# Optimization experiments

Measured on AMD Instinct MI355X. Metric: run time of the kernel, lower is better.

The kernel has to match this reference:

```python
import jax, jax.numpy as jnp
import numpy as np

K = 7            # attention window
HEADS = 8
C_ATT = 32       # in_channels of AttBlock
DKH = C_ATT // HEADS  # 4
C_FC = 512       # resnet18 fc channels
NUM_CLASS = 20


def conv2d(x, w, b, stride=1, padding=0):
    out = jax.lax.conv_general_dilated(
        x, w, (stride, stride), [(padding, padding), (padding, padding)],
        dimension_numbers=("NCHW", "OIHW", "NCHW"))
    return out + b[None, :, None, None]


def unfold2(t, k, H, W):
    # torch t.unfold(2,k,1).unfold(3,k,1): [B,C,Hp,Wp] -> [B,C,H,W,k,k]
    t = jnp.stack([t[:, :, i:i + H, :] for i in range(k)], axis=-1)      # [B,C,H,Wp,k]
    t = jnp.stack([t[:, :, :, j:j + W, :] for j in range(k)], axis=-1)   # [B,C,H,W,k,k]
    return t


def bilinear_resize(x, oh, ow):
    # torch F.interpolate(mode='bilinear', align_corners=False)
    B, C, H, W = x.shape
    ys = jnp.clip((jnp.arange(oh, dtype=x.dtype) + 0.5) * (H / oh) - 0.5, 0, H - 1)
    xs = jnp.clip((jnp.arange(ow, dtype=x.dtype) + 0.5) * (W / ow) - 0.5, 0, W - 1)
    y0 = jnp.floor(ys).astype(jnp.int32); y1 = jnp.minimum(y0 + 1, H - 1)
    x0 = jnp.floor(xs).astype(jnp.int32); x1 = jnp.minimum(x0 + 1, W - 1)
    wy = (ys - y0)[None, None, :, None]
    wx = (xs - x0)[None, None, None, :]
    g = lambda yi, xi: x[:, :, yi][:, :, :, xi]
    top = g(y0, x0) * (1 - wx) + g(y0, x1) * wx
    bot = g(y1, x0) * (1 - wx) + g(y1, x1) * wx
    return top * (1 - wy) + bot * wy


def att_block(x, conv1_w, conv1_b, k_w, k_b, q_w, q_b, v_w, v_b, rel_h, rel_w):
    B, _, H, W = x.shape
    x1 = conv2d(x, conv1_w, conv1_b, padding=1)                    # [B,32,H,W]
    p = (K - 1) // 2
    xp = jnp.pad(x1, ((0, 0), (0, 0), (p, K - 1 - p), (p, K - 1 - p)))
    k = conv2d(xp, k_w, k_b)                                       # [B,32,H+6,W+6]
    q = conv2d(x1, q_w, q_b)                                       # [B,32,H,W]
    v = conv2d(xp, v_w, v_b)
    k = unfold2(k, K, H, W).reshape(B, HEADS, H, W, DKH, -1)       # raw row-major reshape (as torch)
    v = unfold2(v, K, H, W).reshape(B, HEADS, H, W, DKH, -1)
    q = q.reshape(B, HEADS, H, W, DKH, 1)
    qk = jnp.matmul(jnp.swapaxes(q, 4, 5), k).reshape(B, HEADS, H, W, K, K)
    # einsum 'bhxydz,cij->bhxyij' fully contracts d,z,c -> outer product of sums
    qsum = q.sum(axis=(4, 5))                                      # [B,heads,H,W]
    rel = rel_h.sum(0) + rel_w.sum(0)                              # [K,1]+[1,K] -> [K,K]
    qk = qk + qsum[..., None, None] * rel
    w = jax.nn.softmax(qk.reshape(B, HEADS, H, W, 1, K * K), axis=-1)
    attn = jnp.matmul(w, jnp.swapaxes(v, 4, 5))                    # [B,heads,H,W,1,dvh]
    return attn.reshape(B, -1, H, W)                               # [B,32,H,W]


def setup_inputs() -> dict:
    key = jax.random.key(0)
    ks = jax.random.split(key, 16)
    s = 0.05
    inp = {
        "x": jax.random.normal(ks[0], (1, 6, 256, 256), jnp.float32),
        "diff_input": 1,
        "backbone_w": jax.random.normal(ks[1], (C_FC, 6, 3, 3), jnp.float32) * s,
        "backbone_b": jax.random.normal(ks[2], (C_FC,), jnp.float32) * s,
        "conv1_w": jax.random.normal(ks[3], (C_ATT, 6, 3, 3), jnp.float32) * s,
        "conv1_b": jax.random.normal(ks[4], (C_ATT,), jnp.float32) * s,
        "k_w": jax.random.normal(ks[5], (C_ATT, C_ATT, 1, 1), jnp.float32) * s,
        "k_b": jax.random.normal(ks[6], (C_ATT,), jnp.float32) * s,
        "q_w": jax.random.normal(ks[7], (C_ATT, C_ATT, 1, 1), jnp.float32) * s,
        "q_b": jax.random.normal(ks[8], (C_ATT,), jnp.float32) * s,
        "v_w": jax.random.normal(ks[9], (C_ATT, C_ATT, 1, 1), jnp.float32) * s,
        "v_b": jax.random.normal(ks[10], (C_ATT,), jnp.float32) * s,
        "rel_h": jax.random.normal(ks[11], (C_ATT // 2, K, 1), jnp.float32),
        "rel_w": jax.random.normal(ks[12], (C_ATT // 2, 1, K), jnp.float32),
        "expand_w": jax.random.normal(ks[13], (C_FC, C_ATT, 3, 3), jnp.float32) * s,
        "expand_b": jax.random.normal(ks[14], (C_FC,), jnp.float32) * s,
        "fc_w": jax.random.normal(ks[15], (NUM_CLASS, C_FC), jnp.float32) * s,
        "fc_b": jnp.zeros((NUM_CLASS,), jnp.float32),
    }
    return inp


def reference(x, diff_input, backbone_w, backbone_b, conv1_w, conv1_b,
              k_w, k_b, q_w, q_b, v_w, v_b, rel_h, rel_w,
              expand_w, expand_b, fc_w, fc_b):
    # multi_task_model stub: stride-8 conv trunk -> [B,512,H/8,W/8]
    res_out = conv2d(x, backbone_w, backbone_b, stride=8, padding=1)
    # diff_input is not None -> attention branch always taken
    att_res = att_block(x, conv1_w, conv1_b, k_w, k_b, q_w, q_b, v_w, v_b, rel_h, rel_w)
    att_scale = bilinear_resize(att_res, res_out.shape[2], res_out.shape[3])
    att_enhance = res_out + conv2d(att_scale, expand_w, expand_b, padding=1)
    pooled = att_enhance.mean(axis=(2, 3))          # AdaptiveAvgPool2d((1,1))
    fc_x = pooled @ fc_w.T + fc_b                   # [B,num_class]
    return fc_x
```

## Files before the change

kernel.cpp:

```cpp
#include <hip/hip_runtime.h>
#include <math.h>


#define OFF_STATA ((size_t)0)
#define OFF_SX    ((size_t)3072)
#define OFF_G     ((size_t)3136)
#define OFF_GB    ((size_t)8896)
#define OFF_FCB2  ((size_t)9976)

#define SM_KT   0
#define SM_VT   2176
#define SM_QS   4352
#define SM_ML   4864
#define SM_BIAS 5032
#define SM_RW   5040
#define SM_RED  5056
#define SM_TOT  5120

__global__ __launch_bounds__(256) void k_fused(
    const float* __restrict__ x,
    const float* __restrict__ c1w, const float* __restrict__ c1b,
    const float* __restrict__ kw, const float* __restrict__ kb,
    const float* __restrict__ qw, const float* __restrict__ qb,
    const float* __restrict__ vw, const float* __restrict__ vb,
    const float* __restrict__ relh, const float* __restrict__ relw,
    const float* __restrict__ bw, const float* __restrict__ bb,
    const float* __restrict__ ew, const float* __restrict__ eb,
    const float* __restrict__ fcw, const float* __restrict__ fcb,
    float* __restrict__ statA, float* __restrict__ Sx,
    float* __restrict__ G, float* __restrict__ Gb,
    float* __restrict__ FCB2) {
  __shared__ float smem[SM_TOT];
  int tid = threadIdx.x;
  int bid = blockIdx.x;

  if (bid >= 1024) {
    float* red2 = smem;
    if (bid < 1078) {
      int e = bid - 1024;
      int ci = e / 9, rem = e - ci * 9, ky = rem / 3, kx = rem - ky * 3;
      const float* xc = x + (size_t)ci * 65536;
      float acc = 0.f;
      for (int p = tid; p < 1024; p += 256) {
        int oy = p >> 5, ox = p & 31;
        int ry = 8 * oy - 1 + ky, cx = 8 * ox - 1 + kx;
        if (ry >= 0 && ry <= 255 && cx >= 0 && cx <= 255)
          acc += xc[ry * 256 + cx];
      }
      #pragma unroll
      for (int off = 32; off >= 1; off >>= 1) acc += __shfl_down(acc, off);
      if ((tid & 63) == 0) red2[tid >> 6] = acc;
      __syncthreads();
      if (tid == 0) Sx[e] = red2[0] + red2[1] + red2[2] + red2[3];
      return;
    }
    if (bid < 1185) {
      int gi0 = (bid - 1078) * 64;
      int l = tid & 63, w = tid >> 6;
      int g = gi0 + l;
      int o = g / 342;
      int i = g - o * 342;
      bool valid = (g < 6840);
      int oc = valid ? o : 0;
      float acc = 0.f;
      const float* fr = fcw + oc * 512;
      #pragma unroll 8
      for (int mm = 0; mm < 128; ++mm) {
        int m = w * 128 + mm;
        float val = (i < 288) ? ew[m * 288 + i] : bw[m * 54 + (i - 288)];
        acc = fmaf(fr[m], val, acc);
      }
      red2[tid] = acc;
      __syncthreads();
      if (w == 0 && valid) {
        float s = red2[l] + red2[64 + l] + red2[128 + l] + red2[192 + l];
        if (i < 288) G[o * 288 + i] = s;
        else         Gb[o * 54 + (i - 288)] = s;
      }
      return;
    }
    {
      int o = bid - 1185;
      float acc = fmaf(fcw[o * 512 + tid], bb[tid] + eb[tid],
                       fcw[o * 512 + 256 + tid] * (bb[256 + tid] + eb[256 + tid]));
      #pragma unroll
      for (int off = 32; off >= 1; off >>= 1) acc += __shfl_down(acc, off);
      if ((tid & 63) == 0) red2[tid >> 6] = acc;
      __syncthreads();
      if (tid == 0) FCB2[o] = fcb[o] + red2[0] + red2[1] + red2[2] + red2[3];
      return;
    }
  }

  int c  = bid >> 5;
  int oy = bid & 31;

  float* KT  = smem + SM_KT;
  float* VT  = smem + SM_VT;
  float* QS  = smem + SM_QS;
  float* Ml  = smem + SM_ML;
  float* bsl = smem + SM_BIAS;
  float* rhs = smem + SM_RW;
  float* rws = smem + SM_RW + 8;
  float* red = smem + SM_RED;

  if (tid < 168) {
    int ci = tid / 28, s = tid - ci * 28;
    if (s < 27) {
      int kind = s / 9, t9 = s - kind * 9;
      const float* w3 = (kind == 0 ? kw : (kind == 1 ? vw : qw)) + c * 32;
      float a = 0.f;
      #pragma unroll
      for (int m = 0; m < 32; ++m)
        a = fmaf(w3[m], c1w[(m * 6 + ci) * 9 + t9], a);
      Ml[ci * 28 + s] = a;
    }
  } else if (tid < 176) {
    int s = tid - 168;
    if (s < 3) {
      const float* w3 = (s == 0 ? kw : (s == 1 ? vw : qw)) + c * 32;
      float a = (s == 0 ? kb : (s == 1 ? vb : qb))[c];
      #pragma unroll
      for (int m = 0; m < 32; ++m) a = fmaf(w3[m], c1b[m], a);
      bsl[s] = a;
    } else if (s == 3) bsl[3] = kb[c];
    else if (s == 4) bsl[4] = vb[c];
  } else if (tid < 184) {
    int i = tid - 176;
    if (i < 7) {
      float s = 0.f;
      for (int cc = 0; cc < 16; ++cc) s += relh[cc * 7 + i];
      rhs[i] = s;
    }
  } else if (tid < 192) {
    int j = tid - 184;
    if (j < 7) {
      float s = 0.f;
      for (int cc = 0; cc < 16; ++cc) s += relw[cc * 7 + j];
      rws[j] = s;
    }
  }
  __syncthreads();

  int cg = tid & 63, rg = tid >> 6;
  int roq = (rg == 1) ? 1 : ((rg == 2) ? 0 : -1);
  float kacc[2][4], vacc[2][4], qacc[4];
  {
    float mk = bsl[0], mv = bsl[1], mq = bsl[2];
    #pragma unroll
    for (int ro = 0; ro < 2; ++ro)
      #pragma unroll
      for (int cc = 0; cc < 4; ++cc) { kacc[ro][cc] = mk; vacc[ro][cc] = mv; }
    #pragma unroll
    for (int cc = 0; cc < 4; ++cc) qacc[cc] = mq;
  }
  float mA = (cg > 0) ? 1.0f : 0.0f;
  float mC = (cg < 63) ? 1.0f : 0.0f;
  int xr0 = 8 * oy + 2 * rg - 1;

  #pragma unroll 1
  for (int ci = 0; ci < 6; ++ci) {
    const float* xch = x + (size_t)ci * 65536;
    float wch[28];
    {
      const float4* Mc = (const float4*)&Ml[ci * 28];
      *(float4*)&wch[0]  = Mc[0]; *(float4*)&wch[4]  = Mc[1];
      *(float4*)&wch[8]  = Mc[2]; *(float4*)&wch[12] = Mc[3];
      *(float4*)&wch[16] = Mc[4]; *(float4*)&wch[20] = Mc[5];
      *(float4*)&wch[24] = Mc[6];
    }
    #pragma unroll
    for (int s4 = 0; s4 < 4; ++s4) {
      int xr = xr0 + s4;
      if (xr < 0 || xr > 255) continue;
      float4 Bv = *(const float4*)&xch[xr * 256 + 4 * cg];
      float left  = __shfl_up(Bv.w, 1);
      float right = __shfl_down(Bv.x, 1);
      float win[6];
      win[0] = left * mA;
      win[1] = Bv.x;
      win[2] = Bv.y;
      win[3] = Bv.z;
      win[4] = Bv.w;
      win[5] = right * mC;
      if (s4 < 3) {
        const float* wk = &wch[3 * s4];
        const float* wv = &wch[9 + 3 * s4];
        #pragma unroll
        for (int cc = 0; cc < 4; ++cc) {
          float a = kacc[0][cc], b2 = vacc[0][cc];
          #pragma unroll
          for (int dxw = 0; dxw < 3; ++dxw) {
            float xv = win[cc + dxw];
            a  = fmaf(wk[dxw], xv, a);
            b2 = fmaf(wv[dxw], xv, b2);
          }
          kacc[0][cc] = a; vacc[0][cc] = b2;
        }
        if (roq == 0) {
          const float* wq = &wch[18 + 3 * s4];
          #pragma unroll
          for (int cc = 0; cc < 4; ++cc) {
            float qa = qacc[cc];
            #pragma unroll
            for (int dxw = 0; dxw < 3; ++dxw)
              qa = fmaf(wq[dxw], win[cc + dxw], qa);
            qacc[cc] = qa;
          }
        }
      }
      if (s4 >= 1) {
        const float* wk = &wch[3 * (s4 - 1)];
        const float* wv = &wch[9 + 3 * (s4 - 1)];
        #pragma unroll
        for (int cc = 0; cc < 4; ++cc) {
          float a = kacc[1][cc], b2 = vacc[1][cc];
          #pragma unroll
          for (int dxw = 0; dxw < 3; ++dxw) {
            float xv = win[cc + dxw];
            a  = fmaf(wk[dxw], xv, a);
            b2 = fmaf(wv[dxw], xv, b2);
          }
          kacc[1][cc] = a; vacc[1][cc] = b2;
        }
        if (roq == 1) {
          const float* wq = &wch[18 + 3 * (s4 - 1)];
          #pragma unroll
          for (int cc = 0; cc < 4; ++cc) {
            float qa = qacc[cc];
            #pragma unroll
            for (int dxw = 0; dxw < 3; ++dxw)
              qa = fmaf(wq[dxw], win[cc + dxw], qa);
            qacc[cc] = qa;
          }
        }
      }
    }
  }

  #pragma unroll
  for (int ro = 0; ro < 2; ++ro) {
    int r = 2 * rg + ro;
    *(float4*)&KT[r * 272 + 4 * cg + 4] =
        make_float4(kacc[ro][0], kacc[ro][1], kacc[ro][2], kacc[ro][3]);
    *(float4*)&VT[r * 272 + 4 * cg + 4] =
        make_float4(vacc[ro][0], vacc[ro][1], vacc[ro][2], vacc[ro][3]);
  }
  if (roq >= 0)
    *(float4*)&QS[(rg == 2 ? 256 : 0) + 4 * cg] =
        make_float4(qacc[0], qacc[1], qacc[2], qacc[3]);
  if (tid < 96) {
    int t2 = tid;
    int kv = t2 >= 48; if (kv) t2 -= 48;
    int lr = t2 & 7, pi = t2 >> 3;
    int slot = (pi < 3) ? (pi + 1) : (pi + 257);
    (kv ? VT : KT)[lr * 272 + slot] = bsl[3 + kv];
  }
  __syncthreads();

  {
    int half = tid & 1;
    int pix  = tid >> 1;
    int dx   = pix & 1;
    int ox   = (pix >> 1) & 31;
    int dy   = (pix >> 6) & 1;
    int wb   = 8 * ox + 4 * dx;
    int dv   = dx ? 0 : 3;
    int i0   = half * 3;

    float4 qv4 = *(const float4*)&QS[dy * 256 + wb];
    float qv0 = qv4.x, qv1 = qv4.y, qv2 = qv4.z, qv3 = qv4.w;
    float qsum = qv0 + qv1 + qv2 + qv3;

    float sum = 0.f, o = 0.f;
    #pragma unroll
    for (int ii = 0; ii < 4; ++ii) {
      int i = i0 + ii;
      float act = ((half == 0) || (ii > 0)) ? 1.0f : 0.0f;
      const float* kr = &KT[(dy + i) * 272 + wb];
      const float* vr = &VT[(dy + i) * 272 + wb];
      float B[12], BV[12];
      *(float4*)&B[0]  = *(const float4*)&kr[0];
      *(float4*)&B[4]  = *(const float4*)&kr[4];
      *(float4*)&B[8]  = *(const float4*)&kr[8];
      *(float4*)&BV[0] = *(const float4*)&vr[0];
      *(float4*)&BV[4] = *(const float4*)&vr[4];
      *(float4*)&BV[8] = *(const float4*)&vr[8];
      float rh = rhs[i];
      #pragma unroll
      for (int j = 0; j < 7; ++j) {
        float d0 = fmaf(qv0, B[j + 1],
                   fmaf(qv1, B[j + 2],
                   fmaf(qv2, B[j + 3], qv3 * B[j + 4])));
        float s = fmaf(qsum, rh + rws[j], d0);
        float e = act * __expf(s);
        sum += e;
        o = fmaf(e, BV[dv + j + 1], o);
      }
    }
    sum += __shfl_xor(sum, 1);
    o   += __shfl_xor(o, 1);

    float quarter = 0.25f * o / sum;
    float psum = quarter + __shfl_xor(quarter, 2);
    if ((tid & 3) == 0) red[dy * 32 + ox] = psum;
  }
  __syncthreads();

  if (tid < 32) {
    float scv = red[tid] + red[32 + tid];
    float e0  = __shfl(scv, 0, 32);
    float e31 = __shfl(scv, 31, 32);
    float rs = scv;
    #pragma unroll
    for (int off = 16; off >= 1; off >>= 1) rs += __shfl_down(rs, off, 32);
    if (tid == 0) {
      float* pa = statA + (c * 32 + oy) * 3;
      pa[0] = rs; pa[1] = e0; pa[2] = e31;
    }
  }
}

__global__ __launch_bounds__(64) void k_out(
    const float* __restrict__ statA, const float* __restrict__ Sx,
    const float* __restrict__ G, const float* __restrict__ Gb,
    const float* __restrict__ FCB2, float* __restrict__ out) {
  __shared__ float Sl[288];
  __shared__ float SxL[54];
  int o = blockIdx.x, lane = threadIdx.x;
  if (lane < 32) {
    int ch = lane;
    const float* pa = statA + ch * 96;
    float T = 0.f, C0 = 0.f, C31 = 0.f;
    #pragma unroll
    for (int i = 0; i < 32; ++i) {
      T += pa[3 * i]; C0 += pa[3 * i + 1]; C31 += pa[3 * i + 2];
    }
    float r0 = pa[0],  e00 = pa[1],    e0_31 = pa[2];
    float r31 = pa[93], e31_0 = pa[94], e31_31 = pa[95];
    #pragma unroll
    for (int ky = 0; ky < 3; ++ky) {
      float exR = (ky == 0) ? r31 : (ky == 2 ? r0 : 0.f);
      #pragma unroll
      for (int kx = 0; kx < 3; ++kx) {
        float exC = (kx == 0) ? C31 : (kx == 2 ? C0 : 0.f);
        float corner = 0.f;
        if (ky != 1 && kx != 1) {
          if (ky == 0) corner = (kx == 0) ? e31_31 : e31_0;
          else         corner = (kx == 0) ? e0_31  : e00;
        }
        Sl[ch * 9 + ky * 3 + kx] = T - exR - exC + corner;
      }
    }
  } else {
    for (int idx = lane - 32; idx < 54; idx += 32) SxL[idx] = Sx[idx];
  }
  __syncthreads();

  float acc = 0.f;
  #pragma unroll
  for (int i0 = 0; i0 < 288; i0 += 64) {
    int i = i0 + lane;
    if (i < 288) acc = fmaf(G[o * 288 + i], Sl[i], acc);
  }
  if (lane < 54) acc = fmaf(Gb[o * 54 + lane], SxL[lane], acc);
  #pragma unroll
  for (int off = 32; off >= 1; off >>= 1) acc += __shfl_down(acc, off);
  if (lane == 0) out[o] = FCB2[o] + acc * (1.0f / 1024.0f);
}

extern "C" void kernel_launch(void* const* d_in, const int* in_sizes, int n_in,
                              void* d_out, int out_size, void* d_ws, size_t ws_size,
                              hipStream_t stream) {
  const float* x    = (const float*)d_in[0];
  const float* bw   = (const float*)d_in[2];
  const float* bb   = (const float*)d_in[3];
  const float* c1w  = (const float*)d_in[4];
  const float* c1b  = (const float*)d_in[5];
  const float* kw   = (const float*)d_in[6];
  const float* kb   = (const float*)d_in[7];
  const float* qw   = (const float*)d_in[8];
  const float* qb   = (const float*)d_in[9];
  const float* vw   = (const float*)d_in[10];
  const float* vb   = (const float*)d_in[11];
  const float* relh = (const float*)d_in[12];
  const float* relw = (const float*)d_in[13];
  const float* ew   = (const float*)d_in[14];
  const float* eb   = (const float*)d_in[15];
  const float* fcw  = (const float*)d_in[16];
  const float* fcb  = (const float*)d_in[17];

  float* ws    = (float*)d_ws;
  float* statA = ws + OFF_STATA;
  float* Sxb   = ws + OFF_SX;
  float* Gm    = ws + OFF_G;
  float* Gbm   = ws + OFF_GB;
  float* FCB2  = ws + OFF_FCB2;
  float* out   = (float*)d_out;

  k_fused<<<1205, 256, 0, stream>>>(x, c1w, c1b, kw, kb, qw, qb, vw, vb,
                                    relh, relw, bw, bb, ew, eb, fcw, fcb,
                                    statA, Sxb, Gm, Gbm, FCB2);
  k_out  <<<20,   64,  0, stream>>>(statA, Sxb, Gm, Gbm, FCB2, out);
}
```

Before: 29.79 us.

## Double block size to 512 threads, one conv row per wavefront

Raises the fused kernel to 512 threads per block. In the conv phase each wavefront now computes one K/V row instead of two, which removes the two-accumulator register pattern. In the attention phase four threads now share each pixel's window rows instead of two. The shared-memory row stride changes from 272 to 276 and the auxiliary blocks are adjusted for eight waves. The aim is more parallelism per block and fewer serial FMAs per thread. In exchange, neighbouring conv rows now each reload the same input rows, and every block carries more synchronisation and reduction overhead.

```diff
diff --git a/kernel.cpp b/kernel.cpp
--- a/kernel.cpp
+++ b/kernel.cpp
@@ -9,15 +9,15 @@
 #define OFF_FCB2  ((size_t)9976)
 
 #define SM_KT   0
-#define SM_VT   2176
-#define SM_QS   4352
-#define SM_ML   4864
-#define SM_BIAS 5032
-#define SM_RW   5040
-#define SM_RED  5056
-#define SM_TOT  5120
-
-__global__ __launch_bounds__(256) void k_fused(
+#define SM_VT   2208
+#define SM_QS   4416
+#define SM_ML   4928
+#define SM_BIAS 5096
+#define SM_RW   5104
+#define SM_RED  5120
+#define SM_TOT  5184
+
+__global__ __launch_bounds__(512) void k_fused(
     const float* __restrict__ x,
     const float* __restrict__ c1w, const float* __restrict__ c1b,
     const float* __restrict__ kw, const float* __restrict__ kb,
@@ -41,7 +41,7 @@
       int ci = e / 9, rem = e - ci * 9, ky = rem / 3, kx = rem - ky * 3;
       const float* xc = x + (size_t)ci * 65536;
       float acc = 0.f;
-      for (int p = tid; p < 1024; p += 256) {
+      for (int p = tid; p < 1024; p += 512) {
         int oy = p >> 5, ox = p & 31;
         int ry = 8 * oy - 1 + ky, cx = 8 * ox - 1 + kx;
         if (ry >= 0 && ry <= 255 && cx >= 0 && cx <= 255)
@@ -51,7 +51,12 @@
       for (int off = 32; off >= 1; off >>= 1) acc += __shfl_down(acc, off);
       if ((tid & 63) == 0) red2[tid >> 6] = acc;
       __syncthreads();
-      if (tid == 0) Sx[e] = red2[0] + red2[1] + red2[2] + red2[3];
+      if (tid == 0) {
+        float s = 0.f;
+        #pragma unroll
+        for (int wv2 = 0; wv2 < 8; ++wv2) s += red2[wv2];
+        Sx[e] = s;
+      }
       return;
     }
     if (bid < 1185) {
@@ -65,15 +70,17 @@
       float acc = 0.f;
       const float* fr = fcw + oc * 512;
       #pragma unroll 8
-      for (int mm = 0; mm < 128; ++mm) {
-        int m = w * 128 + mm;
+      for (int mm = 0; mm < 64; ++mm) {
+        int m = w * 64 + mm;
         float val = (i < 288) ? ew[m * 288 + i] : bw[m * 54 + (i - 288)];
         acc = fmaf(fr[m], val, acc);
       }
       red2[tid] = acc;
       __syncthreads();
       if (w == 0 && valid) {
-        float s = red2[l] + red2[64 + l] + red2[128 + l] + red2[192 + l];
+        float s = 0.f;
+        #pragma unroll
+        for (int wv2 = 0; wv2 < 8; ++wv2) s += red2[wv2 * 64 + l];
         if (i < 288) G[o * 288 + i] = s;
         else         Gb[o * 54 + (i - 288)] = s;
       }
@@ -81,13 +88,17 @@
     }
     {
       int o = bid - 1185;
-      float acc = fmaf(fcw[o * 512 + tid], bb[tid] + eb[tid],
-                       fcw[o * 512 + 256 + tid] * (bb[256 + tid] + eb[256 + tid]));
+      float acc = fcw[o * 512 + tid] * (bb[tid] + eb[tid]);
       #pragma unroll
       for (int off = 32; off >= 1; off >>= 1) acc += __shfl_down(acc, off);
       if ((tid & 63) == 0) red2[tid >> 6] = acc;
       __syncthreads();
-      if (tid == 0) FCB2[o] = fcb[o] + red2[0] + red2[1] + red2[2] + red2[3];
+      if (tid == 0) {
+        float s = fcb[o];
+        #pragma unroll
+        for (int wv2 = 0; wv2 < 8; ++wv2) s += red2[wv2];
+        FCB2[o] = s;
+      }
       return;
     }
   }
@@ -142,21 +153,17 @@
   }
   __syncthreads();
 
-  int cg = tid & 63, rg = tid >> 6;
-  int roq = (rg == 1) ? 1 : ((rg == 2) ? 0 : -1);
-  float kacc[2][4], vacc[2][4], qacc[4];
+  int cg = tid & 63, r = tid >> 6;
+  bool isq = (r == 3 || r == 4);
+  float kacc[4], vacc[4], qacc[4];
   {
     float mk = bsl[0], mv = bsl[1], mq = bsl[2];
     #pragma unroll
-    for (int ro = 0; ro < 2; ++ro)
-      #pragma unroll
-      for (int cc = 0; cc < 4; ++cc) { kacc[ro][cc] = mk; vacc[ro][cc] = mv; }
-    #pragma unroll
-    for (int cc = 0; cc < 4; ++cc) qacc[cc] = mq;
+    for (int cc = 0; cc < 4; ++cc) { kacc[cc] = mk; vacc[cc] = mv; qacc[cc] = mq; }
   }
   float mA = (cg > 0) ? 1.0f : 0.0f;
   float mC = (cg < 63) ? 1.0f : 0.0f;
-  int xr0 = 8 * oy + 2 * rg - 1;
+  int xrbase = 8 * oy + r - 1;
 
   #pragma unroll 1
   for (int ci = 0; ci < 6; ++ci) {
@@ -170,8 +177,8 @@
       *(float4*)&wch[24] = Mc[6];
     }
     #pragma unroll
-    for (int s4 = 0; s4 < 4; ++s4) {
-      int xr = xr0 + s4;
+    for (int dy = 0; dy < 3; ++dy) {
+      int xr = xrbase + dy;
       if (xr < 0 || xr > 255) continue;
       float4 Bv = *(const float4*)&xch[xr * 256 + 4 * cg];
       float left  = __shfl_up(Bv.w, 1);
@@ -183,90 +190,58 @@
       win[3] = Bv.z;
       win[4] = Bv.w;
       win[5] = right * mC;
-      if (s4 < 3) {
-        const float* wk = &wch[3 * s4];
-        const float* wv = &wch[9 + 3 * s4];
+      const float* wk = &wch[3 * dy];
+      const float* wv = &wch[9 + 3 * dy];
+      #pragma unroll
+      for (int cc = 0; cc < 4; ++cc) {
+        float a = kacc[cc], b2 = vacc[cc];
+        #pragma unroll
+        for (int dxw = 0; dxw < 3; ++dxw) {
+          float xv = win[cc + dxw];
+          a  = fmaf(wk[dxw], xv, a);
+          b2 = fmaf(wv[dxw], xv, b2);
+        }
+        kacc[cc] = a; vacc[cc] = b2;
+      }
+      if (isq) {
+        const float* wq = &wch[18 + 3 * dy];
         #pragma unroll
         for (int cc = 0; cc < 4; ++cc) {
-          float a = kacc[0][cc], b2 = vacc[0][cc];
+          float qa = qacc[cc];
           #pragma unroll
-          for (int dxw = 0; dxw < 3; ++dxw) {
-            float xv = win[cc + dxw];
-            a  = fmaf(wk[dxw], xv, a);
-            b2 = fmaf(wv[dxw], xv, b2);
-          }
-          kacc[0][cc] = a; vacc[0][cc] = b2;
+          for (int dxw = 0; dxw < 3; ++dxw)
+            qa = fmaf(wq[dxw], win[cc + dxw], qa);
+          qacc[cc] = qa;
         }
-        if (roq == 0) {
-          const float* wq = &wch[18 + 3 * s4];
-          #pragma unroll
-          for (int cc = 0; cc < 4; ++cc) {
-            float qa = qacc[cc];
-            #pragma unroll
-            for (int dxw = 0; dxw < 3; ++dxw)
-              qa = fmaf(wq[dxw], win[cc + dxw], qa);
-            qacc[cc] = qa;
-          }
-        }
-      }
-      if (s4 >= 1) {
-        const float* wk = &wch[3 * (s4 - 1)];
-        const float* wv = &wch[9 + 3 * (s4 - 1)];
-        #pragma unroll
-        for (int cc = 0; cc < 4; ++cc) {
-          float a = kacc[1][cc], b2 = vacc[1][cc];
-          #pragma unroll
-          for (int dxw = 0; dxw < 3; ++dxw) {
-            float xv = win[cc + dxw];
-            a  = fmaf(wk[dxw], xv, a);
-            b2 = fmaf(wv[dxw], xv, b2);
-          }
-          kacc[1][cc] = a; vacc[1][cc] = b2;
-        }
-        if (roq == 1) {
-          const float* wq = &wch[18 + 3 * (s4 - 1)];
-          #pragma unroll
-          for (int cc = 0; cc < 4; ++cc) {
-            float qa = qacc[cc];
-            #pragma unroll
-            for (int dxw = 0; dxw < 3; ++dxw)
-              qa = fmaf(wq[dxw], win[cc + dxw], qa);
-            qacc[cc] = qa;
-          }
-        }
-      }
-    }
-  }
-
-  #pragma unroll
-  for (int ro = 0; ro < 2; ++ro) {
-    int r = 2 * rg + ro;
-    *(float4*)&KT[r * 272 + 4 * cg + 4] =
-        make_float4(kacc[ro][0], kacc[ro][1], kacc[ro][2], kacc[ro][3]);
-    *(float4*)&VT[r * 272 + 4 * cg + 4] =
-        make_float4(vacc[ro][0], vacc[ro][1], vacc[ro][2], vacc[ro][3]);
-  }
-  if (roq >= 0)
-    *(float4*)&QS[(rg == 2 ? 256 : 0) + 4 * cg] =
-        make_float4(qacc[0], qacc[1], qacc[2], qacc[3]);
+      }
+    }
+  }
+
+  *(float4*)&KT[r * 276 + 4 * cg + 4] =
+      make_float4(kacc[0], kacc[1], kacc[2], kacc[3]);
+  *(float4*)&VT[r * 276 + 4 * cg + 4] =
+      make_float4(vacc[0], vacc[1], vacc[2], vacc[3]);
+  if (r == 3)
+    *(float4*)&QS[4 * cg] = make_float4(qacc[0], qacc[1], qacc[2], qacc[3]);
+  if (r == 4)
+    *(float4*)&QS[256 + 4 * cg] = make_float4(qacc[0], qacc[1], qacc[2], qacc[3]);
   if (tid < 96) {
     int t2 = tid;
     int kv = t2 >= 48; if (kv) t2 -= 48;
     int lr = t2 & 7, pi = t2 >> 3;
     int slot = (pi < 3) ? (pi + 1) : (pi + 257);
-    (kv ? VT : KT)[lr * 272 + slot] = bsl[3 + kv];
+    (kv ? VT : KT)[lr * 276 + slot] = bsl[3 + kv];
   }
   __syncthreads();
 
   {
-    int half = tid & 1;
-    int pix  = tid >> 1;
+    int quarter = tid & 3;
+    int pix  = tid >> 2;
     int dx   = pix & 1;
     int ox   = (pix >> 1) & 31;
     int dy   = (pix >> 6) & 1;
     int wb   = 8 * ox + 4 * dx;
     int dv   = dx ? 0 : 3;
-    int i0   = half * 3;
 
     float4 qv4 = *(const float4*)&QS[dy * 256 + wb];
     float qv0 = qv4.x, qv1 = qv4.y, qv2 = qv4.z, qv3 = qv4.w;
@@ -274,11 +249,12 @@
 
     float sum = 0.f, o = 0.f;
     #pragma unroll
-    for (int ii = 0; ii < 4; ++ii) {
-      int i = i0 + ii;
-      float act = ((half == 0) || (ii > 0)) ? 1.0f : 0.0f;
-      const float* kr = &KT[(dy + i) * 272 + wb];
-      const float* vr = &VT[(dy + i) * 272 + wb];
+    for (int ii = 0; ii < 2; ++ii) {
+      int i = quarter + 4 * ii;
+      float act = (i < 7) ? 1.0f : 0.0f;
+      int irow = (i < 7) ? i : 0;
+      const float* kr = &KT[(dy + irow) * 276 + wb];
+      const float* vr = &VT[(dy + irow) * 276 + wb];
       float B[12], BV[12];
       *(float4*)&B[0]  = *(const float4*)&kr[0];
       *(float4*)&B[4]  = *(const float4*)&kr[4];
@@ -286,7 +262,7 @@
       *(float4*)&BV[0] = *(const float4*)&vr[0];
       *(float4*)&BV[4] = *(const float4*)&vr[4];
       *(float4*)&BV[8] = *(const float4*)&vr[8];
-      float rh = rhs[i];
+      float rh = rhs[irow];
       #pragma unroll
       for (int j = 0; j < 7; ++j) {
         float d0 = fmaf(qv0, B[j + 1],
@@ -300,10 +276,12 @@
     }
     sum += __shfl_xor(sum, 1);
     o   += __shfl_xor(o, 1);
-
-    float quarter = 0.25f * o / sum;
-    float psum = quarter + __shfl_xor(quarter, 2);
-    if ((tid & 3) == 0) red[dy * 32 + ox] = psum;
+    sum += __shfl_xor(sum, 2);
+    o   += __shfl_xor(o, 2);
+
+    float quarterv = 0.25f * o / sum;
+    float psum = quarterv + __shfl_xor(quarterv, 4);
+    if ((tid & 7) == 0) red[dy * 32 + ox] = psum;
   }
   __syncthreads();
 
@@ -398,7 +376,7 @@
   float* FCB2  = ws + OFF_FCB2;
   float* out   = (float*)d_out;
 
-  k_fused<<<1205, 256, 0, stream>>>(x, c1w, c1b, kw, kb, qw, qb, vw, vb,
+  k_fused<<<1205, 512, 0, stream>>>(x, c1w, c1b, kw, kb, qw, qb, vw, vb,
                                     relh, relw, bw, bb, ew, eb, fcw, fcb,
                                     statA, Sxb, Gm, Gbm, FCB2);
   k_out  <<<20,   64,  0, stream>>>(statA, Sxb, Gm, Gbm, FCB2, out);
```

Result: slower. 31.35 us (+5.2%).

## Fuse final output kernel into main kernel via last-block atomic counter

Applied to the files above, without the earlier changes.

Removes the separate k_out launch. Each block of k_fused now increments a global counter after a threadfence, and the last block to finish does the final reduction over statA, Sx, G and Gb for all 20 outputs. This saves a kernel launch and the gap between kernels. In exchange it adds a memset before the launch, an atomic and fences in every block, and a serialized tail on one block.

```diff
diff --git a/kernel.cpp b/kernel.cpp
--- a/kernel.cpp
+++ b/kernel.cpp
@@ -7,6 +7,7 @@
 #define OFF_G     ((size_t)3136)
 #define OFF_GB    ((size_t)8896)
 #define OFF_FCB2  ((size_t)9976)
+#define OFF_CNT   ((size_t)10000)
 
 #define SM_KT   0
 #define SM_VT   2176
@@ -29,8 +30,10 @@
     const float* __restrict__ fcw, const float* __restrict__ fcb,
     float* __restrict__ statA, float* __restrict__ Sx,
     float* __restrict__ G, float* __restrict__ Gb,
-    float* __restrict__ FCB2) {
+    float* __restrict__ FCB2, unsigned int* __restrict__ cnt,
+    float* __restrict__ out) {
   __shared__ float smem[SM_TOT];
+  __shared__ unsigned int rankS;
   int tid = threadIdx.x;
   int bid = blockIdx.x;
 
@@ -52,9 +55,7 @@
       if ((tid & 63) == 0) red2[tid >> 6] = acc;
       __syncthreads();
       if (tid == 0) Sx[e] = red2[0] + red2[1] + red2[2] + red2[3];
-      return;
-    }
-    if (bid < 1185) {
+    } else if (bid < 1185) {
       int gi0 = (bid - 1078) * 64;
       int l = tid & 63, w = tid >> 6;
       int g = gi0 + l;
@@ -77,9 +78,7 @@
         if (i < 288) G[o * 288 + i] = s;
         else         Gb[o * 54 + (i - 288)] = s;
       }
-      return;
-    }
-    {
+    } else {
       int o = bid - 1185;
       float acc = fmaf(fcw[o * 512 + tid], bb[tid] + eb[tid],
                        fcw[o * 512 + 256 + tid] * (bb[256 + tid] + eb[256 + tid]));
@@ -88,248 +87,248 @@
       if ((tid & 63) == 0) red2[tid >> 6] = acc;
       __syncthreads();
       if (tid == 0) FCB2[o] = fcb[o] + red2[0] + red2[1] + red2[2] + red2[3];
-      return;
-    }
-  }
-
-  int c  = bid >> 5;
-  int oy = bid & 31;
-
-  float* KT  = smem + SM_KT;
-  float* VT  = smem + SM_VT;
-  float* QS  = smem + SM_QS;
-  float* Ml  = smem + SM_ML;
-  float* bsl = smem + SM_BIAS;
-  float* rhs = smem + SM_RW;
-  float* rws = smem + SM_RW + 8;
-  float* red = smem + SM_RED;
-
-  if (tid < 168) {
-    int ci = tid / 28, s = tid - ci * 28;
-    if (s < 27) {
-      int kind = s / 9, t9 = s - kind * 9;
-      const float* w3 = (kind == 0 ? kw : (kind == 1 ? vw : qw)) + c * 32;
-      float a = 0.f;
-      #pragma unroll
-      for (int m = 0; m < 32; ++m)
-        a = fmaf(w3[m], c1w[(m * 6 + ci) * 9 + t9], a);
-      Ml[ci * 28 + s] = a;
-    }
-  } else if (tid < 176) {
-    int s = tid - 168;
-    if (s < 3) {
-      const float* w3 = (s == 0 ? kw : (s == 1 ? vw : qw)) + c * 32;
-      float a = (s == 0 ? kb : (s == 1 ? vb : qb))[c];
-      #pragma unroll
-      for (int m = 0; m < 32; ++m) a = fmaf(w3[m], c1b[m], a);
-      bsl[s] = a;
-    } else if (s == 3) bsl[3] = kb[c];
-    else if (s == 4) bsl[4] = vb[c];
-  } else if (tid < 184) {
-    int i = tid - 176;
-    if (i < 7) {
-      float s = 0.f;
-      for (int cc = 0; cc < 16; ++cc) s += relh[cc * 7 + i];
-      rhs[i] = s;
-    }
-  } else if (tid < 192) {
-    int j = tid - 184;
-    if (j < 7) {
-      float s = 0.f;
-      for (int cc = 0; cc < 16; ++cc) s += relw[cc * 7 + j];
-      rws[j] = s;
-    }
-  }
-  __syncthreads();
-
-  int cg = tid & 63, rg = tid >> 6;
-  int roq = (rg == 1) ? 1 : ((rg == 2) ? 0 : -1);
-  float kacc[2][4], vacc[2][4], qacc[4];
-  {
-    float mk = bsl[0], mv = bsl[1], mq = bsl[2];
-    #pragma unroll
-    for (int ro = 0; ro < 2; ++ro)
-      #pragma unroll
-      for (int cc = 0; cc < 4; ++cc) { kacc[ro][cc] = mk; vacc[ro][cc] = mv; }
-    #pragma unroll
-    for (int cc = 0; cc < 4; ++cc) qacc[cc] = mq;
-  }
-  float mA = (cg > 0) ? 1.0f : 0.0f;
-  float mC = (cg < 63) ? 1.0f : 0.0f;
-  int xr0 = 8 * oy + 2 * rg - 1;
-
-  #pragma unroll 1
-  for (int ci = 0; ci < 6; ++ci) {
-    const float* xch = x + (size_t)ci * 65536;
-    float wch[28];
+    }
+  } else {
+    int c  = bid >> 5;
+    int oy = bid & 31;
+
+    float* KT  = smem + SM_KT;
+    float* VT  = smem + SM_VT;
+    float* QS  = smem + SM_QS;
+    float* Ml  = smem + SM_ML;
+    float* bsl = smem + SM_BIAS;
+    float* rhs = smem + SM_RW;
+    float* rws = smem + SM_RW + 8;
+    float* red = smem + SM_RED;
+
+    if (tid < 168) {
+      int ci = tid / 28, s = tid - ci * 28;
+      if (s < 27) {
+        int kind = s / 9, t9 = s - kind * 9;
+        const float* w3 = (kind == 0 ? kw : (kind == 1 ? vw : qw)) + c * 32;
+        float a = 0.f;
+        #pragma unroll
+        for (int m = 0; m < 32; ++m)
+          a = fmaf(w3[m], c1w[(m * 6 + ci) * 9 + t9], a);
+        Ml[ci * 28 + s] = a;
+      }
+    } else if (tid < 176) {
+      int s = tid - 168;
+      if (s < 3) {
+        const float* w3 = (s == 0 ? kw : (s == 1 ? vw : qw)) + c * 32;
+        float a = (s == 0 ? kb : (s == 1 ? vb : qb))[c];
+        #pragma unroll
+        for (int m = 0; m < 32; ++m) a = fmaf(w3[m], c1b[m], a);
+        bsl[s] = a;
+      } else if (s == 3) bsl[3] = kb[c];
+      else if (s == 4) bsl[4] = vb[c];
+    } else if (tid < 184) {
+      int i = tid - 176;
+      if (i < 7) {
+        float s = 0.f;
+        for (int cc = 0; cc < 16; ++cc) s += relh[cc * 7 + i];
+        rhs[i] = s;
+      }
+    } else if (tid < 192) {
+      int j = tid - 184;
+      if (j < 7) {
+        float s = 0.f;
+        for (int cc = 0; cc < 16; ++cc) s += relw[cc * 7 + j];
+        rws[j] = s;
+      }
+    }
+    __syncthreads();
+
+    int cg = tid & 63, rg = tid >> 6;
+    int roq = (rg == 1) ? 1 : ((rg == 2) ? 0 : -1);
+    float kacc[2][4], vacc[2][4], qacc[4];
     {
-      const float4* Mc = (const float4*)&Ml[ci * 28];
-      *(float4*)&wch[0]  = Mc[0]; *(float4*)&wch[4]  = Mc[1];
-      *(float4*)&wch[8]  = Mc[2]; *(float4*)&wch[12] = Mc[3];
-      *(float4*)&wch[16] = Mc[4]; *(float4*)&wch[20] = Mc[5];
-      *(float4*)&wch[24] = Mc[6];
-    }
-    #pragma unroll
-    for (int s4 = 0; s4 < 4; ++s4) {
-      int xr = xr0 + s4;
-      if (xr < 0 || xr > 255) continue;
-      float4 Bv = *(const float4*)&xch[xr * 256 + 4 * cg];
-      float left  = __shfl_up(Bv.w, 1);
-      float right = __shfl_down(Bv.x, 1);
-      float win[6];
-      win[0] = left * mA;
-      win[1] = Bv.x;
-      win[2] = Bv.y;
-      win[3] = Bv.z;
-      win[4] = Bv.w;
-      win[5] = right * mC;
-      if (s4 < 3) {
-        const float* wk = &wch[3 * s4];
-        const float* wv = &wch[9 + 3 * s4];
+      float mk = bsl[0], mv = bsl[1], mq = bsl[2];
+      #pragma unroll
+      for (int ro = 0; ro < 2; ++ro)
         #pragma unroll
-        for (int cc = 0; cc < 4; ++cc) {
-          float a = kacc[0][cc], b2 = vacc[0][cc];
-          #pragma unroll
-          for (int dxw = 0; dxw < 3; ++dxw) {
-            float xv = win[cc + dxw];
-            a  = fmaf(wk[dxw], xv, a);
-            b2 = fmaf(wv[dxw], xv, b2);
-          }
-          kacc[0][cc] = a; vacc[0][cc] = b2;
-        }
-        if (roq == 0) {
-          const float* wq = &wch[18 + 3 * s4];
+        for (int cc = 0; cc < 4; ++cc) { kacc[ro][cc] = mk; vacc[ro][cc] = mv; }
+      #pragma unroll
+      for (int cc = 0; cc < 4; ++cc) qacc[cc] = mq;
+    }
+    float mA = (cg > 0) ? 1.0f : 0.0f;
+    float mC = (cg < 63) ? 1.0f : 0.0f;
+    int xr0 = 8 * oy + 2 * rg - 1;
+
+    #pragma unroll 1
+    for (int ci = 0; ci < 6; ++ci) {
+      const float* xch = x + (size_t)ci * 65536;
+      float wch[28];
+      {
+        const float4* Mc = (const float4*)&Ml[ci * 28];
+        *(float4*)&wch[0]  = Mc[0]; *(float4*)&wch[4]  = Mc[1];
+        *(float4*)&wch[8]  = Mc[2]; *(float4*)&wch[12] = Mc[3];
+        *(float4*)&wch[16] = Mc[4]; *(float4*)&wch[20] = Mc[5];
+        *(float4*)&wch[24] = Mc[6];
+      }
+      #pragma unroll
+      for (int s4 = 0; s4 < 4; ++s4) {
+        int xr = xr0 + s4;
+        if (xr < 0 || xr > 255) continue;
+        float4 Bv = *(const float4*)&xch[xr * 256 + 4 * cg];
+        float left  = __shfl_up(Bv.w, 1);
+        float right = __shfl_down(Bv.x, 1);
+        float win[6];
+        win[0] = left * mA;
+        win[1] = Bv.x;
+        win[2] = Bv.y;
+        win[3] = Bv.z;
+        win[4] = Bv.w;
+        win[5] = right * mC;
+        if (s4 < 3) {
+          const float* wk = &wch[3 * s4];
+          const float* wv = &wch[9 + 3 * s4];
           #pragma unroll
           for (int cc = 0; cc < 4; ++cc) {
-            float qa = qacc[cc];
+            float a = kacc[0][cc], b2 = vacc[0][cc];
             #pragma unroll
-            for (int dxw = 0; dxw < 3; ++dxw)
-              qa = fmaf(wq[dxw], win[cc + dxw], qa);
-            qacc[cc] = qa;
+            for (int dxw = 0; dxw < 3; ++dxw) {
+              float xv = win[cc + dxw];
+              a  = fmaf(wk[dxw], xv, a);
+              b2 = fmaf(wv[dxw], xv, b2);
+            }
+            kacc[0][cc] = a; vacc[0][cc] = b2;
+          }
+          if (roq == 0) {
+            const float* wq = &wch[18 + 3 * s4];
+            #pragma unroll
+            for (int cc = 0; cc < 4; ++cc) {
+              float qa = qacc[cc];
+              #pragma unroll
+              for (int dxw = 0; dxw < 3; ++dxw)
+                qa = fmaf(wq[dxw], win[cc + dxw], qa);
+              qacc[cc] = qa;
+            }
           }
         }
-      }
-      if (s4 >= 1) {
-        const float* wk = &wch[3 * (s4 - 1)];
-        const float* wv = &wch[9 + 3 * (s4 - 1)];
-        #pragma unroll
-        for (int cc = 0; cc < 4; ++cc) {
-          float a = kacc[1][cc], b2 = vacc[1][cc];
-          #pragma unroll
-          for (int dxw = 0; dxw < 3; ++dxw) {
-            float xv = win[cc + dxw];
-            a  = fmaf(wk[dxw], xv, a);
-            b2 = fmaf(wv[dxw], xv, b2);
-          }
-          kacc[1][cc] = a; vacc[1][cc] = b2;
-        }
-        if (roq == 1) {
-          const float* wq = &wch[18 + 3 * (s4 - 1)];
+        if (s4 >= 1) {
+          const float* wk = &wch[3 * (s4 - 1)];
+          const float* wv = &wch[9 + 3 * (s4 - 1)];
           #pragma unroll
           for (int cc = 0; cc < 4; ++cc) {
-            float qa = qacc[cc];
+            float a = kacc[1][cc], b2 = vacc[1][cc];
             #pragma unroll
-            for (int dxw = 0; dxw < 3; ++dxw)
-              qa = fmaf(wq[dxw], win[cc + dxw], qa);
-            qacc[cc] = qa;
+            for (int dxw = 0; dxw < 3; ++dxw) {
+              float xv = win[cc + dxw];
+              a  = fmaf(wk[dxw], xv, a);
+              b2 = fmaf(wv[dxw], xv, b2);
+            }
+            kacc[1][cc] = a; vacc[1][cc] = b2;
+          }
+          if (roq == 1) {
+            const float* wq = &wch[18 + 3 * (s4 - 1)];
+            #pragma unroll
+            for (int cc = 0; cc < 4; ++cc) {
+              float qa = qacc[cc];
+              #pragma unroll
+              for (int dxw = 0; dxw < 3; ++dxw)
+                qa = fmaf(wq[dxw], win[cc + dxw], qa);
+              qacc[cc] = qa;
+            }
           }
         }
       }
     }
+
+    #pragma unroll
+    for (int ro = 0; ro < 2; ++ro) {
+      int r = 2 * rg + ro;
+      *(float4*)&KT[r * 272 + 4 * cg + 4] =
+          make_float4(kacc[ro][0], kacc[ro][1], kacc[ro][2], kacc[ro][3]);
+      *(float4*)&VT[r * 272 + 4 * cg + 4] =
+          make_float4(vacc[ro][0], vacc[ro][1], vacc[ro][2], vacc[ro][3]);
+    }
+    if (roq >= 0)
+      *(float4*)&QS[(rg == 2 ? 256 : 0) + 4 * cg] =
+          make_float4(qacc[0], qacc[1], qacc[2], qacc[3]);
+    if (tid < 96) {
+      int t2 = tid;
+      int kv = t2 >= 48; if (kv) t2 -= 48;
+      int lr = t2 & 7, pi = t2 >> 3;
+      int slot = (pi < 3) ? (pi + 1) : (pi + 257);
+      (kv ? VT : KT)[lr * 272 + slot] = bsl[3 + kv];
+    }
+    __syncthreads();
+
+    {
+      int half = tid & 1;
+      int pix  = tid >> 1;
+      int dx   = pix & 1;
+      int ox   = (pix >> 1) & 31;
+      int dy   = (pix >> 6) & 1;
+      int wb   = 8 * ox + 4 * dx;
+      int dv   = dx ? 0 : 3;
+      int i0   = half * 3;
+
+      float4 qv4 = *(const float4*)&QS[dy * 256 + wb];
+      float qv0 = qv4.x, qv1 = qv4.y, qv2 = qv4.z, qv3 = qv4.w;
+      float qsum = qv0 + qv1 + qv2 + qv3;
+
+      float sum = 0.f, o = 0.f;
+      #pragma unroll
+      for (int ii = 0; ii < 4; ++ii) {
+        int i = i0 + ii;
+        float act = ((half == 0) || (ii > 0)) ? 1.0f : 0.0f;
+        const float* kr = &KT[(dy + i) * 272 + wb];
+        const float* vr = &VT[(dy + i) * 272 + wb];
+        float B[12], BV[12];
+        *(float4*)&B[0]  = *(const float4*)&kr[0];
+        *(float4*)&B[4]  = *(const float4*)&kr[4];
+        *(float4*)&B[8]  = *(const float4*)&kr[8];
+        *(float4*)&BV[0] = *(const float4*)&vr[0];
+        *(float4*)&BV[4] = *(const float4*)&vr[4];
+        *(float4*)&BV[8] = *(const float4*)&vr[8];
+        float rh = rhs[i];
+        #pragma unroll
+        for (int j = 0; j < 7; ++j) {
+          float d0 = fmaf(qv0, B[j + 1],
+                     fmaf(qv1, B[j + 2],
+                     fmaf(qv2, B[j + 3], qv3 * B[j + 4])));
+          float s = fmaf(qsum, rh + rws[j], d0);
+          float e = act * __expf(s);
+          sum += e;
+          o = fmaf(e, BV[dv + j + 1], o);
+        }
+      }
+      sum += __shfl_xor(sum, 1);
+      o   += __shfl_xor(o, 1);
+
+      float quarter = 0.25f * o / sum;
+      float psum = quarter + __shfl_xor(quarter, 2);
+      if ((tid & 3) == 0) red[dy * 32 + ox] = psum;
+    }
+    __syncthreads();
+
+    if (tid < 32) {
+      float scv = red[tid] + red[32 + tid];
+      float e0  = __shfl(scv, 0, 32);
+      float e31 = __shfl(scv, 31, 32);
+      float rs = scv;
+      #pragma unroll
+      for (int off = 16; off >= 1; off >>= 1) rs += __shfl_down(rs, off, 32);
+      if (tid == 0) {
+        float* pa = statA + (c * 32 + oy) * 3;
+        pa[0] = rs; pa[1] = e0; pa[2] = e31;
+      }
+    }
   }
 
-  #pragma unroll
-  for (int ro = 0; ro < 2; ++ro) {
-    int r = 2 * rg + ro;
-    *(float4*)&KT[r * 272 + 4 * cg + 4] =
-        make_float4(kacc[ro][0], kacc[ro][1], kacc[ro][2], kacc[ro][3]);
-    *(float4*)&VT[r * 272 + 4 * cg + 4] =
-        make_float4(vacc[ro][0], vacc[ro][1], vacc[ro][2], vacc[ro][3]);
-  }
-  if (roq >= 0)
-    *(float4*)&QS[(rg == 2 ? 256 : 0) + 4 * cg] =
-        make_float4(qacc[0], qacc[1], qacc[2], qacc[3]);
-  if (tid < 96) {
-    int t2 = tid;
-    int kv = t2 >= 48; if (kv) t2 -= 48;
-    int lr = t2 & 7, pi = t2 >> 3;
-    int slot = (pi < 3) ? (pi + 1) : (pi + 257);
-    (kv ? VT : KT)[lr * 272 + slot] = bsl[3 + kv];
-  }
   __syncthreads();
-
-  {
-    int half = tid & 1;
-    int pix  = tid >> 1;
-    int dx   = pix & 1;
-    int ox   = (pix >> 1) & 31;
-    int dy   = (pix >> 6) & 1;
-    int wb   = 8 * ox + 4 * dx;
-    int dv   = dx ? 0 : 3;
-    int i0   = half * 3;
-
-    float4 qv4 = *(const float4*)&QS[dy * 256 + wb];
-    float qv0 = qv4.x, qv1 = qv4.y, qv2 = qv4.z, qv3 = qv4.w;
-    float qsum = qv0 + qv1 + qv2 + qv3;
-
-    float sum = 0.f, o = 0.f;
-    #pragma unroll
-    for (int ii = 0; ii < 4; ++ii) {
-      int i = i0 + ii;
-      float act = ((half == 0) || (ii > 0)) ? 1.0f : 0.0f;
-      const float* kr = &KT[(dy + i) * 272 + wb];
-      const float* vr = &VT[(dy + i) * 272 + wb];
-      float B[12], BV[12];
-      *(float4*)&B[0]  = *(const float4*)&kr[0];
-      *(float4*)&B[4]  = *(const float4*)&kr[4];
-      *(float4*)&B[8]  = *(const float4*)&kr[8];
-      *(float4*)&BV[0] = *(const float4*)&vr[0];
-      *(float4*)&BV[4] = *(const float4*)&vr[4];
-      *(float4*)&BV[8] = *(const float4*)&vr[8];
-      float rh = rhs[i];
-      #pragma unroll
-      for (int j = 0; j < 7; ++j) {
-        float d0 = fmaf(qv0, B[j + 1],
-                   fmaf(qv1, B[j + 2],
-                   fmaf(qv2, B[j + 3], qv3 * B[j + 4])));
-        float s = fmaf(qsum, rh + rws[j], d0);
-        float e = act * __expf(s);
-        sum += e;
-        o = fmaf(e, BV[dv + j + 1], o);
-      }
-    }
-    sum += __shfl_xor(sum, 1);
-    o   += __shfl_xor(o, 1);
-
-    float quarter = 0.25f * o / sum;
-    float psum = quarter + __shfl_xor(quarter, 2);
-    if ((tid & 3) == 0) red[dy * 32 + ox] = psum;
-  }
+  __threadfence();
+  if (tid == 0) rankS = atomicAdd(cnt, 1u);
   __syncthreads();
-
+  if (rankS != 1204u) return;
+  __threadfence();
+
+  float* Sl  = smem;
+  float* SxL = smem + 288;
   if (tid < 32) {
-    float scv = red[tid] + red[32 + tid];
-    float e0  = __shfl(scv, 0, 32);
-    float e31 = __shfl(scv, 31, 32);
-    float rs = scv;
-    #pragma unroll
-    for (int off = 16; off >= 1; off >>= 1) rs += __shfl_down(rs, off, 32);
-    if (tid == 0) {
-      float* pa = statA + (c * 32 + oy) * 3;
-      pa[0] = rs; pa[1] = e0; pa[2] = e31;
-    }
-  }
-}
-
-__global__ __launch_bounds__(64) void k_out(
-    const float* __restrict__ statA, const float* __restrict__ Sx,
-    const float* __restrict__ G, const float* __restrict__ Gb,
-    const float* __restrict__ FCB2, float* __restrict__ out) {
-  __shared__ float Sl[288];
-  __shared__ float SxL[54];
-  int o = blockIdx.x, lane = threadIdx.x;
-  if (lane < 32) {
-    int ch = lane;
+    int ch = tid;
     const float* pa = statA + ch * 96;
     float T = 0.f, C0 = 0.f, C31 = 0.f;
     #pragma unroll
@@ -352,21 +351,26 @@
         Sl[ch * 9 + ky * 3 + kx] = T - exR - exC + corner;
       }
     }
-  } else {
-    for (int idx = lane - 32; idx < 54; idx += 32) SxL[idx] = Sx[idx];
+  } else if (tid >= 64 && tid < 118) {
+    SxL[tid - 64] = Sx[tid - 64];
   }
   __syncthreads();
 
-  float acc = 0.f;
-  #pragma unroll
-  for (int i0 = 0; i0 < 288; i0 += 64) {
-    int i = i0 + lane;
-    if (i < 288) acc = fmaf(G[o * 288 + i], Sl[i], acc);
+  int w = tid >> 6, lane = tid & 63;
+  #pragma unroll 1
+  for (int oo = 0; oo < 5; ++oo) {
+    int o = w * 5 + oo;
+    float acc = 0.f;
+    #pragma unroll
+    for (int i0 = 0; i0 < 288; i0 += 64) {
+      int i = i0 + lane;
+      if (i < 288) acc = fmaf(G[o * 288 + i], Sl[i], acc);
+    }
+    if (lane < 54) acc = fmaf(Gb[o * 54 + lane], SxL[lane], acc);
+    #pragma unroll
+    for (int off = 32; off >= 1; off >>= 1) acc += __shfl_down(acc, off);
+    if (lane == 0) out[o] = FCB2[o] + acc * (1.0f / 1024.0f);
   }
-  if (lane < 54) acc = fmaf(Gb[o * 54 + lane], SxL[lane], acc);
-  #pragma unroll
-  for (int off = 32; off >= 1; off >>= 1) acc += __shfl_down(acc, off);
-  if (lane == 0) out[o] = FCB2[o] + acc * (1.0f / 1024.0f);
 }
 
 extern "C" void kernel_launch(void* const* d_in, const int* in_sizes, int n_in,
@@ -396,10 +400,11 @@
   float* Gm    = ws + OFF_G;
   float* Gbm   = ws + OFF_GB;
   float* FCB2  = ws + OFF_FCB2;
+  unsigned int* cnt = (unsigned int*)(ws + OFF_CNT);
   float* out   = (float*)d_out;
 
+  hipMemsetAsync(cnt, 0, sizeof(unsigned int), stream);
   k_fused<<<1205, 256, 0, stream>>>(x, c1w, c1b, kw, kb, qw, qb, vw, vb,
                                     relh, relw, bw, bb, ew, eb, fcw, fcb,
-                                    statA, Sxb, Gm, Gbm, FCB2);
-  k_out  <<<20,   64,  0, stream>>>(statA, Sxb, Gm, Gbm, FCB2, out);
+                                    statA, Sxb, Gm, Gbm, FCB2, cnt, out);
 }
```

After: 104.5 us. 3.51x slower.
